# Optimization experiments

Measured on AMD Instinct MI355X. Metric: run time of the kernel, lower is better.

The kernel has to match this reference:

```python
import jax, jax.numpy as jnp
import numpy as np

BS, T, C, H, W = 2, 3, 256, 48, 48
NH, NP, NL = 8, 4, 3
DH = C // NH
HW = H * W
LQ = T * HW


def conv2d(x, w, b):
    # x: (N,C,H,W), w: (O,I,3,3), padding=1 (SAME)
    y = jax.lax.conv_general_dilated(x, w, (1, 1), 'SAME',
                                     dimension_numbers=('NCHW', 'OIHW', 'NCHW'))
    return y + b[None, :, None, None]


def grid_sample(img, grid, align_corners, padding_mode):
    # img: (B,C,Hi,Wi); grid: (B,Hg,Wg,2) in [-1,1], last dim = (x,y)
    B, Ch, Hi, Wi = img.shape
    gx, gy = grid[..., 0], grid[..., 1]
    if align_corners:
        x = (gx + 1.0) * 0.5 * (Wi - 1)
        y = (gy + 1.0) * 0.5 * (Hi - 1)
    else:
        x = ((gx + 1.0) * Wi - 1.0) * 0.5
        y = ((gy + 1.0) * Hi - 1.0) * 0.5
    if padding_mode == 'border':
        x = jnp.clip(x, 0.0, Wi - 1)
        y = jnp.clip(y, 0.0, Hi - 1)
    x0 = jnp.floor(x); y0 = jnp.floor(y)
    x1 = x0 + 1.0; y1 = y0 + 1.0
    wx1 = x - x0; wx0 = 1.0 - wx1
    wy1 = y - y0; wy0 = 1.0 - wy1
    imgf = img.reshape(B, Ch, Hi * Wi)

    def gather(xi, yi):
        xc = jnp.clip(xi, 0, Wi - 1).astype(jnp.int32)
        yc = jnp.clip(yi, 0, Hi - 1).astype(jnp.int32)
        flat = (yc * Wi + xc).reshape(B, 1, -1)
        g = jnp.take_along_axis(imgf, flat, axis=2).reshape(B, Ch, *xi.shape[1:])
        if padding_mode == 'zeros':
            valid = ((xi >= 0) & (xi <= Wi - 1) & (yi >= 0) & (yi <= Hi - 1))
            g = g * valid[:, None].astype(img.dtype)
        return g

    out = (gather(x0, y0) * (wx0 * wy0)[:, None]
           + gather(x1, y0) * (wx1 * wy0)[:, None]
           + gather(x0, y1) * (wx0 * wy1)[:, None]
           + gather(x1, y1) * (wx1 * wy1)[:, None])
    return out


def warp(x, flo):
    # x: (B,C,H,W), flo: (B,2,H,W) pixel flow; border padding, align_corners=True
    B, Ch, Hh, Ww = x.shape
    gy, gx = jnp.meshgrid(jnp.arange(Hh), jnp.arange(Ww), indexing='ij')
    grid = jnp.stack([gx, gy], 0).astype(x.dtype)[None]  # (1,2,H,W)
    v = grid + flo
    vx = 2.0 * v[:, 0] / max(Ww - 1, 1) - 1.0
    vy = 2.0 * v[:, 1] / max(Hh - 1, 1) - 1.0
    g = jnp.stack([vx, vy], -1)  # (B,H,W,2)
    return grid_sample(x, g, align_corners=True, padding_mode='border')


def flow_guid_offset(flow_forward, flow_backward, off, h, w):
    # off: (N, LQ, NH, NL, NP, 2) -> add frame-to-frame flows per (query level, key level)
    N = off.shape[0]
    hw = h * w
    off = off.reshape(N, NL, hw, NH, NL, NP, 2)
    f01 = flow_forward[:, 0]; f12 = flow_forward[:, 1]
    f02 = f01 + warp(f12, f01)
    b10 = flow_backward[:, 0]; b21 = flow_backward[:, 1]
    b20 = b21 + warp(b10, b21)

    def flat(f):
        return f.transpose(0, 2, 3, 1).reshape(N, hw, 2)

    f01, f12, f02, b10, b21, b20 = map(flat, (f01, f12, f02, b10, b21, b20))
    z = jnp.zeros_like(f01)
    add = jnp.stack([
        jnp.stack([z, f01, f02], axis=2),
        jnp.stack([b10, z, f12], axis=2),
        jnp.stack([b20, b21, z], axis=2)], axis=1)  # (N, 3, hw, 3, 2)
    off = off + add[:, :, :, None, :, None, :]
    return off.reshape(N, NL * hw, NH, NL, NP, 2)


def setup_inputs():
    key = jax.random.key(0)
    ks = jax.random.split(key, 12)
    query = jax.random.normal(ks[0], (BS, T, C, H, W), dtype=jnp.float32)
    input_flatten = jax.random.normal(ks[1], (BS, T, C, H, W), dtype=jnp.float32)
    reference_points = jax.random.uniform(ks[2], (BS, LQ, NL, 2), dtype=jnp.float32)
    input_spatial_shapes = jnp.array([[H, W]] * NL, dtype=jnp.int32)
    input_level_start_index = jnp.array([0, HW, 2 * HW], dtype=jnp.int32)
    input_padding_mask = jnp.zeros((BS, LQ), dtype=bool)
    flow_forward = 3.0 * jax.random.normal(ks[3], (BS, 2, 2, H, W), dtype=jnp.float32)
    flow_backward = 3.0 * jax.random.normal(ks[4], (BS, 2, 2, H, W), dtype=jnp.float32)
    # sampling_offsets bias init (as in _reset_parameters)
    thetas = np.arange(NH) * (2.0 * np.pi / NH)
    g = np.stack([np.cos(thetas), np.sin(thetas)], -1)
    g = g / np.abs(g).max(-1, keepdims=True)
    g = np.tile(g.reshape(NH, 1, 1, 2), (1, NL, NP, 1))
    g = g * (np.arange(NP) + 1).reshape(1, 1, NP, 1)
    b_off = jnp.asarray(g.reshape(-1), dtype=jnp.float32)
    fan = 1.0 / np.sqrt(C * 9)
    w_off = 0.01 * jax.random.normal(ks[5], (NH * NL * NP * 2, C, 3, 3), dtype=jnp.float32)
    w_attn = 0.01 * jax.random.normal(ks[6], (NH * NL * NP, C, 3, 3), dtype=jnp.float32)
    b_attn = jnp.zeros((NH * NL * NP,), dtype=jnp.float32)
    w_val = fan * jax.random.normal(ks[7], (C, C, 3, 3), dtype=jnp.float32)
    b_val = jnp.zeros((C,), dtype=jnp.float32)
    w_out = fan * jax.random.normal(ks[8], (C, C, 3, 3), dtype=jnp.float32)
    b_out = jnp.zeros((C,), dtype=jnp.float32)
    return {'query': query, 'reference_points': reference_points,
            'input_flatten': input_flatten,
            'input_spatial_shapes': input_spatial_shapes,
            'input_level_start_index': input_level_start_index,
            'input_padding_mask': input_padding_mask,
            'flow_forward': flow_forward, 'flow_backward': flow_backward,
            'w_off': w_off, 'b_off': b_off, 'w_attn': w_attn, 'b_attn': b_attn,
            'w_val': w_val, 'b_val': b_val, 'w_out': w_out, 'b_out': b_out}


def reference(query, reference_points, input_flatten, input_spatial_shapes,
              input_level_start_index, input_padding_mask, flow_forward,
              flow_backward, w_off, b_off, w_attn, b_attn, w_val, b_val,
              w_out, b_out):
    bs, t, c, h, w = query.shape
    q2d = query.reshape(bs * t, c, h, w)
    value = conv2d(input_flatten.reshape(bs * t, c, h, w), w_val, b_val)
    off = conv2d(q2d, w_off, b_off)
    attn = conv2d(q2d, w_attn, b_attn)

    def to_seq(x2d, ch):
        return x2d.reshape(bs, t, ch, h * w).transpose(0, 1, 3, 2).reshape(bs, t * h * w, ch)

    value = to_seq(value, c)
    off = to_seq(off, NH * NL * NP * 2)
    attn = to_seq(attn, NH * NL * NP)
    value = jnp.where(input_padding_mask[..., None], 0.0, value)
    value = value.reshape(bs, t * h * w, NH, DH)
    off = off.reshape(bs, LQ, NH, NL, NP, 2)
    off = flow_guid_offset(flow_forward, flow_backward, off, h, w)
    attn = jax.nn.softmax(attn.reshape(bs, LQ, NH, NL * NP), axis=-1)
    attn = attn.reshape(bs, LQ, NH, NL, NP)
    # offset normalizer: (W_l, H_l) per level
    norm = jnp.stack([input_spatial_shapes[:, 1], input_spatial_shapes[:, 0]], -1).astype(off.dtype)
    loc = reference_points[:, :, None, :, None, :] + off / norm[None, None, None, :, None, :]
    grids = 2.0 * loc - 1.0  # (bs, LQ, NH, NL, NP, 2)
    # values per level -> (NL*bs*NH, DH, h, w)
    v = value.reshape(bs, NL, h, w, NH, DH).transpose(1, 0, 4, 5, 2, 3).reshape(NL * bs * NH, DH, h, w)
    g = grids.transpose(3, 0, 2, 1, 4, 5).reshape(NL * bs * NH, LQ, NP, 2)
    sampled = grid_sample(v, g, align_corners=False, padding_mode='zeros')  # (NL*bs*NH, DH, LQ, NP)
    sampled = sampled.reshape(NL, bs, NH, DH, LQ, NP)
    out = jnp.einsum('lnhdqp,nqhlp->nqhd', sampled, attn).reshape(bs, LQ, c)
    out = out.reshape(bs, t, h * w, c).transpose(0, 1, 3, 2).reshape(bs * t, c, h, w)
    return conv2d(out, w_out, b_out)
```

## Files before the change

kernel.cpp:

```cpp
#include <hip/hip_runtime.h>
#include <hip/hip_bf16.h>

#define BS   2
#define T    3
#define CCH  256
#define HH   48
#define WW   48
#define NH   8
#define NP   4
#define NL   3
#define DH   32
#define HWP  (HH*WW)
#define LQ   (T*HWP)
#define NIMG (BS*T)

typedef short v8s __attribute__((ext_vector_type(8)));
typedef float v4f __attribute__((ext_vector_type(4)));
typedef float v2f __attribute__((ext_vector_type(2)));
typedef unsigned int v2u __attribute__((ext_vector_type(2)));
typedef unsigned int v4u __attribute__((ext_vector_type(4)));

__device__ __forceinline__ unsigned short f2b(float f) {
    unsigned u = __float_as_uint(f);
    return (unsigned short)((u + 0x7FFFu + ((u >> 16) & 1u)) >> 16);
}

#define GLOAD_LDS16(gp, lp) \
    __builtin_amdgcn_global_load_lds((const __attribute__((address_space(1))) unsigned int*)(const void*)(gp), \
                                     (__attribute__((address_space(3))) unsigned int*)(void*)(lp), 16, 0, 0)

#define LDS_SLAB  32768
#define LDS_ZROW  69632
#define LDS_TOTAL 69760

__device__ __forceinline__ int xcd_swz(int p, int n) {
    int q = n >> 3, r = n & 7;
    int xcd = p & 7, j = p >> 3;
    return (xcd < r ? xcd * (q + 1) : r * (q + 1) + (xcd - r) * q) + j;
}

#define NB_FLOW 18
#define NB_WCVT 800
#define NB_TCVT 6912
#define WP0 (256*256)
#define WP1 (288*256)

__global__ __launch_bounds__(256) void prep_kernel(
    const float* __restrict__ ff, const float* __restrict__ fb,
    float* __restrict__ addb,
    const float* __restrict__ w_val, const float* __restrict__ w_off,
    const float* __restrict__ w_attn, const float* __restrict__ w_out,
    unsigned short* __restrict__ Wb_val, unsigned short* __restrict__ Wb_oa,
    unsigned short* __restrict__ Wb_out,
    const float* __restrict__ inputf, const float* __restrict__ query,
    unsigned short* __restrict__ inb_v, unsigned short* __restrict__ inb_q)
{
    __shared__ float lds[32][33];
    const int b = blockIdx.x;
    const int tid = threadIdx.x;

    if (b < NB_FLOW) {
        int idx = b * 256 + tid;
        int n = idx / HWP, pix = idx % HWP;
        int y = pix / WW, x = pix % WW;

        auto F = [&](const float* base, int i, int c, int p) {
            return base[n * (2*2*HWP) + i * (2*HWP) + c * HWP + p];
        };

        float f01x = F(ff,0,0,pix), f01y = F(ff,0,1,pix);
        float f12x = F(ff,1,0,pix), f12y = F(ff,1,1,pix);
        float b10x = F(fb,0,0,pix), b10y = F(fb,0,1,pix);
        float b21x = F(fb,1,0,pix), b21y = F(fb,1,1,pix);

        auto bil = [&](const float* base, int i, float fx, float fy, float* ox, float* oy) {
            float vx = (float)x + fx;
            float vy = (float)y + fy;
            float gx = 2.0f * vx / (float)(WW - 1) - 1.0f;
            float gy = 2.0f * vy / (float)(HH - 1) - 1.0f;
            float px = (gx + 1.0f) * 0.5f * (float)(WW - 1);
            float py = (gy + 1.0f) * 0.5f * (float)(HH - 1);
            px = fminf(fmaxf(px, 0.0f), (float)(WW - 1));
            py = fminf(fmaxf(py, 0.0f), (float)(HH - 1));
            float x0f = floorf(px), y0f = floorf(py);
            float wx1 = px - x0f, wx0 = 1.0f - wx1;
            float wy1 = py - y0f, wy0 = 1.0f - wy1;
            int xi0 = (int)x0f, yi0 = (int)y0f;
            int xc0 = min(max(xi0, 0), WW-1), xc1 = min(max(xi0+1, 0), WW-1);
            int yc0 = min(max(yi0, 0), HH-1), yc1 = min(max(yi0+1, 0), HH-1);
            float r[2];
            #pragma unroll
            for (int c = 0; c < 2; ++c) {
                float v00 = F(base, i, c, yc0*WW + xc0);
                float v10 = F(base, i, c, yc0*WW + xc1);
                float v01 = F(base, i, c, yc1*WW + xc0);
                float v11 = F(base, i, c, yc1*WW + xc1);
                r[c] = v00*(wx0*wy0) + v10*(wx1*wy0) + v01*(wx0*wy1) + v11*(wx1*wy1);
            }
            *ox = r[0]; *oy = r[1];
        };

        float wfx, wfy; bil(ff, 1, f01x, f01y, &wfx, &wfy);
        float f02x = f01x + wfx, f02y = f01y + wfy;
        float wbx, wby; bil(fb, 0, b21x, b21y, &wbx, &wby);
        float b20x = b21x + wbx, b20y = b21y + wby;

        float* A = addb + n * (3*HWP*6) + pix * 6;
        const int TS = HWP * 6;
        A[0] = 0.f;   A[1] = 0.f;   A[2] = f01x; A[3] = f01y; A[4] = f02x; A[5] = f02y;
        A[TS+0] = b10x; A[TS+1] = b10y; A[TS+2] = 0.f; A[TS+3] = 0.f; A[TS+4] = f12x; A[TS+5] = f12y;
        A[2*TS+0] = b20x; A[2*TS+1] = b20y; A[2*TS+2] = b21x; A[2*TS+3] = b21y; A[2*TS+4] = 0.f; A[2*TS+5] = 0.f;
    } else if (b < NB_FLOW + NB_WCVT) {
        int idx = (b - NB_FLOW) * 256 + tid;
        if (idx < WP0) {
            int oc = idx >> 8, ic = idx & 255;
            const float* sp = w_val + ((size_t)oc * 256 + ic) * 9;
            #pragma unroll
            for (int j = 0; j < 9; ++j)
                Wb_val[(size_t)j * WP0 + oc * 256 + ic] = f2b(sp[j]);
        } else if (idx < WP0 + WP1) {
            int p3 = idx - WP0;
            int oc = p3 >> 8, ic = p3 & 255;
            const float* sp = (oc < 192)
                ? (w_off  + ((size_t)oc * 256 + ic) * 9)
                : (w_attn + ((size_t)(oc - 192) * 256 + ic) * 9);
            #pragma unroll
            for (int j = 0; j < 9; ++j)
                Wb_oa[(size_t)j * WP1 + oc * 256 + ic] = f2b(sp[j]);
        } else {
            int p3 = idx - WP0 - WP1;
            int oc = p3 >> 8, ic = p3 & 255;
            const float* sp = w_out + ((size_t)oc * 256 + ic) * 9;
            #pragma unroll
            for (int j = 0; j < 9; ++j)
                Wb_out[(size_t)j * WP0 + oc * 256 + ic] = f2b(sp[j]);
        }
    } else {
        int rem = b - NB_FLOW - NB_WCVT;
        int which = rem / 3456;
        int r2 = rem % 3456;
        int px0 = (r2 % 72) * 32;
        int ic0 = ((r2 / 72) % 8) * 32;
        int img = r2 / (72 * 8);
        const float* src = which ? query : inputf;
        unsigned short* dst = which ? inb_q : inb_v;
        #pragma unroll
        for (int s = 0; s < 4; ++s) {
            int icl = (tid >> 5) + s * 8, pxl = tid & 31;
            lds[icl][pxl] = src[((size_t)img * 256 + ic0 + icl) * HWP + px0 + pxl];
        }
        __syncthreads();
        #pragma unroll
        for (int s = 0; s < 4; ++s) {
            int pxl = (tid >> 5) + s * 8, icl = tid & 31;
            dst[((size_t)img * HWP + px0 + pxl) * 256 + ic0 + icl] = f2b(lds[icl][pxl]);
        }
    }
}

template<int NM>
__device__ __forceinline__ void conv_body(
    int cls, int s, int c_lo, int c_hi,
    const char* inIc, const char* Wbc, int Mpad, int oc0, int pxb, int img,
    const float* bias_a, const float* bias_off, const float* bias_attn,
    unsigned short* Vout, float* offb, float* attnb, float* outp,
    const unsigned char* mask, char* lds)
{
    const int tid  = threadIdx.x;
    const int lane = tid & 63;
    const int wv   = tid >> 6;

    const int r0   = pxb / 48;
    const int rlo  = (r0 > 0) ? (r0 - 1) : 0;
    const int pxlo = rlo * 48;

    const int lrow8 = lane >> 3;
    const int lcol  = lane & 7;

    const int rowl = lane & 15;
    const int g    = lane >> 4;
    const int keyx = (rowl & 7) << 4;
    const int aoff0 = ((wv >> 1) * (16 * NM) + rowl) * 128;
    const int pxw   = pxb + (wv & 1) * 64;
    int ypx[4], xpx[4];
    #pragma unroll
    for (int p = 0; p < 4; ++p) {
        int px = pxw + p * 16 + rowl;
        ypx[p] = px / 48;
        xpx[p] = px % 48;
    }
    int ocr_[NM];
    #pragma unroll
    for (int j = 0; j < NM; ++j) ocr_[j] = j * 32 + wv * 8 + lrow8;

    v4f acc[NM][4];
    #pragma unroll
    for (int m = 0; m < NM; ++m)
        #pragma unroll
        for (int p = 0; p < 4; ++p)
            #pragma unroll
            for (int e = 0; e < 4; ++e) acc[m][p][e] = 0.f;

    for (int c = c_lo; c < c_hi; ++c) {
        const int ic0b = c * 128;

        #pragma unroll
        for (int rr = 0; rr < 9; ++rr) {
            int pe  = rr * 32 + wv * 8 + lrow8;
            int gpx = pxlo + pe;
            if (gpx > 2303) gpx = 2303;
            GLOAD_LDS16(inIc + (size_t)gpx * 512 + ic0b + ((lcol ^ (pe & 7)) << 4),
                        lds + LDS_SLAB + (rr * 32 + wv * 8) * 128);
        }
        #pragma unroll
        for (int j = 0; j < NM; ++j) {
            GLOAD_LDS16(Wbc + (size_t)(oc0 + ocr_[j]) * 512 + ic0b + ((lcol ^ (ocr_[j] & 7)) << 4),
                        lds + (j * 32 + wv * 8) * 128);
        }
        asm volatile("s_waitcnt vmcnt(0) lgkmcnt(0)" ::: "memory");
        __builtin_amdgcn_s_barrier();

        for (int k = 0; k < 9; ++k) {
            const int dy = k / 3 - 1, dx = k % 3 - 1;
            const int cur = k & 1;
            if (k < 8) {
                const char* wk1 = Wbc + (size_t)(k + 1) * Mpad * 512;
                #pragma unroll
                for (int j = 0; j < NM; ++j) {
                    GLOAD_LDS16(wk1 + (size_t)(oc0 + ocr_[j]) * 512 + ic0b + ((lcol ^ (ocr_[j] & 7)) << 4),
                                lds + (cur ^ 1) * 16384 + (j * 32 + wv * 8) * 128);
                }
                if (NM == 4) { asm volatile("s_waitcnt vmcnt(4)" ::: "memory"); }
                else         { asm volatile("s_waitcnt vmcnt(3)" ::: "memory"); }
            } else {
                asm volatile("s_waitcnt vmcnt(0)" ::: "memory");
            }
            __builtin_amdgcn_s_barrier();

            int bbase[4], bkey[4];
            #pragma unroll
            for (int p = 0; p < 4; ++p) {
                int ys = ypx[p] + dy, xs = xpx[p] + dx;
                bool val = ((unsigned)ys < 48u) && ((unsigned)xs < 48u);
                int pe = ys * 48 + xs - pxlo;
                bbase[p] = val ? (LDS_SLAB + pe * 128) : LDS_ZROW;
                bkey[p]  = val ? ((pe & 7) << 4) : 0;
            }

            #pragma unroll
            for (int kk = 0; kk < 2; ++kk) {
                const int col = kk * 64 + g * 16;
                v8s a[NM], bfr[4];
                #pragma unroll
                for (int m = 0; m < NM; ++m)
                    a[m] = *(const v8s*)(lds + cur * 16384 + aoff0 + m * 2048 + (col ^ keyx));
                #pragma unroll
                for (int p = 0; p < 4; ++p)
                    bfr[p] = *(const v8s*)(lds + bbase[p] + (col ^ bkey[p]));
                #pragma unroll
                for (int m = 0; m < NM; ++m)
                    #pragma unroll
                    for (int p = 0; p < 4; ++p)
                        acc[m][p] = __builtin_amdgcn_mfma_f32_16x16x32_bf16(a[m], bfr[p], acc[m][p], 0, 0, 0);
            }
            __builtin_amdgcn_s_barrier();
        }
    }

    const int n = img / T, t = img % T;
    const int ocw = oc0 + (wv >> 1) * (16 * NM);

    #pragma unroll
    for (int p = 0; p < 4; ++p) {
        const int px_f = pxw + p * 16 + rowl;
        const int q = t * HWP + px_f;
        bool mk = (cls == 0) ? (mask[n * LQ + q] != 0) : false;
        #pragma unroll
        for (int m = 0; m < NM; ++m) {
            const int oc_f = ocw + m * 16 + g * 4;
            if (cls == 0) {
                unsigned short o[4];
                #pragma unroll
                for (int r = 0; r < 4; ++r) {
                    float v = acc[m][p][r] + bias_a[oc_f + r];
                    if (mk) v = 0.f;
                    o[r] = f2b(v);
                }
                int head = oc_f >> 5, d0 = oc_f & 31;
                v2u pk;
                pk[0] = (unsigned)o[0] | ((unsigned)o[1] << 16);
                pk[1] = (unsigned)o[2] | ((unsigned)o[3] << 16);
                *(v2u*)(Vout + (((size_t)(t * BS + n) * NH + head) * HWP + px_f) * 32 + d0) = pk;
            } else if (cls == 1) {
                if (oc_f < 192) {
                    v4f v;
                    #pragma unroll
                    for (int r = 0; r < 4; ++r) v[r] = acc[m][p][r] + bias_off[oc_f + r];
                    *(v4f*)(offb + ((size_t)n * LQ + q) * 192 + oc_f) = v;
                } else {
                    v4f v;
                    #pragma unroll
                    for (int r = 0; r < 4; ++r) v[r] = acc[m][p][r] + bias_attn[oc_f - 192 + r];
                    *(v4f*)(attnb + ((size_t)n * LQ + q) * 96 + (oc_f - 192)) = v;
                }
            } else {
                #pragma unroll
                for (int r = 0; r < 4; ++r) {
                    float v = acc[m][p][r] + ((s == 0) ? bias_a[oc_f + r] : 0.f);
                    atomicAdd(&outp[((size_t)img * CCH + oc_f + r) * HWP + px_f], v);
                }
            }
        }
    }
}

__global__ __launch_bounds__(256) void convbig(
    int phase,
    const unsigned short* __restrict__ in_a,
    const unsigned short* __restrict__ in_b,
    const unsigned short* __restrict__ Wb_a,
    const unsigned short* __restrict__ Wb_b,
    const float* __restrict__ bias_a,
    const float* __restrict__ bias_off,
    const float* __restrict__ bias_attn,
    unsigned short* __restrict__ Vout,
    float* __restrict__ offb,
    float* __restrict__ attnb,
    float* __restrict__ outp,
    const unsigned char* __restrict__ mask)
{
    __shared__ __align__(16) char lds[LDS_TOTAL];

    const int tid = threadIdx.x;
    if (tid < 8) {
        v8s z;
        #pragma unroll
        for (int j = 0; j < 8; ++j) z[j] = 0;
        *(v8s*)(lds + LDS_ZROW + tid * 16) = z;
    }

    const int p_phys = blockIdx.x;
    int b;
    if (p_phys < 216) b = xcd_swz(p_phys, 216);
    else if (phase == 0) b = 216 + xcd_swz(p_phys - 216, 324);
    else b = 216 + xcd_swz(p_phys - 216, 216);

    int cls, mt, nt, img, Mpad, c_lo, c_hi, s, oc0;
    const unsigned short *inb, *Wb;
    if (phase == 0) {
        s = 0; c_lo = 0; c_hi = 4;
        if (b < 216) { cls = 0; mt = b % 2; int r = b / 2; nt = r % 18; img = r / 18;
                       inb = in_a; Wb = Wb_a; Mpad = 256; oc0 = mt * 128; }
        else { b -= 216; cls = 1; mt = b % 3; int r = b / 3; nt = r % 18; img = r / 18;
               inb = in_b; Wb = Wb_b; Mpad = 288; oc0 = mt * 96; }
    } else {
        cls = 3; s = b / 216; b = b % 216;
        c_lo = 2 * s; c_hi = c_lo + 2;
        mt = b % 2; int r = b / 2; nt = r % 18; img = r / 18;
        inb = in_a; Wb = Wb_a; Mpad = 256; oc0 = mt * 128;
    }

    const int pxb = nt * 128;
    const char* inIc = (const char*)(inb + (size_t)img * HWP * 256);
    const char* Wbc  = (const char*)Wb;

    if (cls == 1) {
        conv_body<3>(cls, s, c_lo, c_hi, inIc, Wbc, Mpad, oc0, pxb, img,
                     bias_a, bias_off, bias_attn, Vout, offb, attnb, outp, mask, lds);
    } else {
        conv_body<4>(cls, s, c_lo, c_hi, inIc, Wbc, Mpad, oc0, pxb, img,
                     bias_a, bias_off, bias_attn, Vout, offb, attnb, outp, mask, lds);
    }
}

__global__ __launch_bounds__(256) void sample_kernel(
    const unsigned short* __restrict__ V,
    const float* __restrict__ offb,
    const float* __restrict__ attnb,
    const float* __restrict__ addb,
    const float* __restrict__ refp,
    unsigned short* __restrict__ midb)
{
    const int tid = threadIdx.x;
    const int gid = tid >> 2, li = tid & 3;
    const int lb = xcd_swz(blockIdx.x, (BS * LQ * NH) / 64);
    const int pair = lb * 64 + gid;
    const int head = pair & 7;
    const int nq = pair >> 3;
    const int n = nq / LQ, q = nq % LQ;
    const int t = q / HWP, pix = q % HWP;

    const float* al = attnb + ((size_t)n * LQ + q) * 96 + head * 12;
    float lg[12];
    {
        v4f t0 = *(const v4f*)al, t1 = *(const v4f*)(al + 4), t2 = *(const v4f*)(al + 8);
        #pragma unroll
        for (int j = 0; j < 4; ++j) { lg[j] = t0[j]; lg[4+j] = t1[j]; lg[8+j] = t2[j]; }
    }
    const float* ofp = offb + ((size_t)n * LQ + q) * 192 + head * 24;
    float of[24];
    #pragma unroll
    for (int j = 0; j < 6; ++j) {
        v4f v = *(const v4f*)(ofp + j * 4);
        #pragma unroll
        for (int e = 0; e < 4; ++e) of[j*4+e] = v[e];
    }
    const float* rpp = refp + ((size_t)n * LQ + q) * 6;
    const float* adp = addb + ((size_t)n * 3 * HWP + t * HWP + pix) * 6;
    float rp[6], ad[6];
    #pragma unroll
    for (int j = 0; j < 3; ++j) {
        v2f r = *(const v2f*)(rpp + j * 2);
        v2f a = *(const v2f*)(adp + j * 2);
        rp[j*2] = r[0]; rp[j*2+1] = r[1];
        ad[j*2] = a[0]; ad[j*2+1] = a[1];
    }

    float m = lg[0];
    #pragma unroll
    for (int j = 1; j < 12; ++j) m = fmaxf(m, lg[j]);
    float s = 0.f;
    #pragma unroll
    for (int j = 0; j < 12; ++j) { lg[j] = expf(lg[j] - m); s += lg[j]; }
    float inv = 1.0f / s;
    #pragma unroll
    for (int j = 0; j < 12; ++j) lg[j] *= inv;

    float acc[8];
    #pragma unroll
    for (int e = 0; e < 8; ++e) acc[e] = 0.f;

    #pragma unroll
    for (int l = 0; l < 3; ++l) {
        float refx = rp[l*2+0], refy = rp[l*2+1];
        float addx = ad[l*2+0], addy = ad[l*2+1];
        const unsigned short* Vi =
            V + (size_t)((l * BS + n) * NH + head) * HWP * DH + li * 8;
        #pragma unroll
        for (int p = 0; p < 4; ++p) {
            float ox = of[(l*4+p)*2+0] + addx;
            float oy = of[(l*4+p)*2+1] + addy;
            float locx = refx + ox * (1.0f/48.0f);
            float locy = refy + oy * (1.0f/48.0f);
            float gx = 2.0f*locx - 1.0f;
            float gy = 2.0f*locy - 1.0f;
            float pxf = ((gx + 1.0f) * 48.0f - 1.0f) * 0.5f;
            float pyf = ((gy + 1.0f) * 48.0f - 1.0f) * 0.5f;
            float x0f = floorf(pxf), y0f = floorf(pyf);
            float wx1 = pxf - x0f, wx0 = 1.0f - wx1;
            float wy1 = pyf - y0f, wy0 = 1.0f - wy1;
            int xi0 = (int)x0f, yi0 = (int)y0f;
            bool vx0 = (x0f >= 0.0f)     && (x0f <= 47.0f);
            bool vx1 = (x0f+1.f >= 0.0f) && (x0f+1.f <= 47.0f);
            bool vy0 = (y0f >= 0.0f)     && (y0f <= 47.0f);
            bool vy1 = (y0f+1.f >= 0.0f) && (y0f+1.f <= 47.0f);
            int xc0 = min(max(xi0, 0), 47),   xc1 = min(max(xi0+1, 0), 47);
            int yc0 = min(max(yi0, 0), 47),   yc1 = min(max(yi0+1, 0), 47);
            float aw = lg[l*4+p];
            float w00 = (vx0 && vy0) ? wx0*wy0*aw : 0.f;
            float w10 = (vx1 && vy0) ? wx1*wy0*aw : 0.f;
            float w01 = (vx0 && vy1) ? wx0*wy1*aw : 0.f;
            float w11 = (vx1 && vy1) ? wx1*wy1*aw : 0.f;
            v4u u00 = *(const v4u*)(Vi + (yc0*WW + xc0)*DH);
            v4u u10 = *(const v4u*)(Vi + (yc0*WW + xc1)*DH);
            v4u u01 = *(const v4u*)(Vi + (yc1*WW + xc0)*DH);
            v4u u11 = *(const v4u*)(Vi + (yc1*WW + xc1)*DH);
            #pragma unroll
            for (int cc = 0; cc < 4; ++cc) {
                v4u u = (cc == 0) ? u00 : (cc == 1) ? u10 : (cc == 2) ? u01 : u11;
                float w = (cc == 0) ? w00 : (cc == 1) ? w10 : (cc == 2) ? w01 : w11;
                #pragma unroll
                for (int e = 0; e < 4; ++e) {
                    acc[e*2+0] += w * __uint_as_float(u[e] << 16);
                    acc[e*2+1] += w * __uint_as_float(u[e] & 0xFFFF0000u);
                }
            }
        }
    }

    v4u pk;
    #pragma unroll
    for (int e = 0; e < 4; ++e)
        pk[e] = (unsigned)f2b(acc[e*2+0]) | ((unsigned)f2b(acc[e*2+1]) << 16);
    *(v4u*)(midb + ((size_t)(n * T + t) * HWP + pix) * 256 + head * 32 + li * 8) = pk;
}

extern "C" void kernel_launch(void* const* d_in, const int* in_sizes, int n_in,
                              void* d_out, int out_size, void* d_ws, size_t ws_size,
                              hipStream_t stream) {
    const float* query  = (const float*)d_in[0];
    const float* refp   = (const float*)d_in[1];
    const float* inputf = (const float*)d_in[2];
    const unsigned char* mask = (const unsigned char*)d_in[5];
    const float* ff     = (const float*)d_in[6];
    const float* fb     = (const float*)d_in[7];
    const float* w_off  = (const float*)d_in[8];
    const float* b_off  = (const float*)d_in[9];
    const float* w_attn = (const float*)d_in[10];
    const float* b_attn = (const float*)d_in[11];
    const float* w_val  = (const float*)d_in[12];
    const float* b_val  = (const float*)d_in[13];
    const float* w_out  = (const float*)d_in[14];
    const float* b_out  = (const float*)d_in[15];

    char* w = (char*)d_ws;
    float* offb  = (float*)w;           w += (size_t)BS*LQ*192*4;
    float* attnb = (float*)w;           w += (size_t)BS*LQ*96*4;
    float* addb  = (float*)w;           w += (size_t)BS*3*HWP*6*4;
    unsigned short* V      = (unsigned short*)w; w += (size_t)48*HWP*DH*2;
    unsigned short* inb_q  = (unsigned short*)w; w += (size_t)NIMG*HWP*256*2;
    unsigned short* inb_v  = (unsigned short*)w; w += (size_t)NIMG*HWP*256*2;
    unsigned short* midb   = inb_v;
    unsigned short* Wb_val = (unsigned short*)w; w += (size_t)9*256*256*2;
    unsigned short* Wb_oa  = (unsigned short*)w; w += (size_t)9*288*256*2;
    unsigned short* Wb_out = (unsigned short*)w; w += (size_t)9*256*256*2;
    float* outp = (float*)d_out;

    hipMemsetAsync(outp, 0, (size_t)NIMG * CCH * HWP * 4, stream);

    prep_kernel<<<NB_FLOW + NB_WCVT + NB_TCVT, 256, 0, stream>>>(
        ff, fb, addb, w_val, w_off, w_attn, w_out,
        Wb_val, Wb_oa, Wb_out, inputf, query, inb_v, inb_q);

    convbig<<<540, 256, 0, stream>>>(0, inb_v, inb_q, Wb_val, Wb_oa,
                                     b_val, b_off, b_attn,
                                     V, offb, attnb, nullptr, mask);

    sample_kernel<<<(BS*LQ*NH)/64, 256, 0, stream>>>(V, offb, attnb, addb, refp, midb);

    convbig<<<432, 256, 0, stream>>>(1, midb, nullptr, Wb_out, nullptr,
                                     b_out, nullptr, nullptr,
                                     nullptr, nullptr, nullptr, outp, nullptr);
}
```

Baseline: 139.5 us.

## Pre-pack conv weights in MFMA fragment order and load A operands directly from global

```diff
diff --git a/kernel.cpp b/kernel.cpp
--- a/kernel.cpp
+++ b/kernel.cpp
@@ -29,9 +29,8 @@
     __builtin_amdgcn_global_load_lds((const __attribute__((address_space(1))) unsigned int*)(const void*)(gp), \
                                      (__attribute__((address_space(3))) unsigned int*)(void*)(lp), 16, 0, 0)
 
-#define LDS_SLAB  32768
-#define LDS_ZROW  69632
-#define LDS_TOTAL 69760
+#define LDS_ZROW  36864
+#define LDS_TOTAL 36992
 
 __device__ __forceinline__ int xcd_swz(int p, int n) {
     int q = n >> 3, r = n & 7;
@@ -44,6 +43,16 @@
 #define NB_TCVT 6912
 #define WP0 (256*256)
 #define WP1 (288*256)
+
+__device__ __forceinline__ void wfrag_store(
+    unsigned short* dst, int Mp, int oc, int ic, int k, float v)
+{
+    int c = ic >> 6, kk = (ic >> 5) & 1, g = (ic >> 3) & 3, j8 = ic & 7;
+    int rowl = oc & 15, ob = oc >> 4;
+    int lane = (g << 4) | rowl;
+    size_t idx = ((((size_t)(k * 4 + c) * (Mp >> 4) + ob) * 2 + kk) * 64 + lane) * 8 + j8;
+    dst[idx] = f2b(v);
+}
 
 __global__ __launch_bounds__(256) void prep_kernel(
     const float* __restrict__ ff, const float* __restrict__ fb,
@@ -117,7 +126,7 @@
             const float* sp = w_val + ((size_t)oc * 256 + ic) * 9;
             #pragma unroll
             for (int j = 0; j < 9; ++j)
-                Wb_val[(size_t)j * WP0 + oc * 256 + ic] = f2b(sp[j]);
+                wfrag_store(Wb_val, 256, oc, ic, j, sp[j]);
         } else if (idx < WP0 + WP1) {
             int p3 = idx - WP0;
             int oc = p3 >> 8, ic = p3 & 255;
@@ -126,14 +135,14 @@
                 : (w_attn + ((size_t)(oc - 192) * 256 + ic) * 9);
             #pragma unroll
             for (int j = 0; j < 9; ++j)
-                Wb_oa[(size_t)j * WP1 + oc * 256 + ic] = f2b(sp[j]);
+                wfrag_store(Wb_oa, 288, oc, ic, j, sp[j]);
         } else {
             int p3 = idx - WP0 - WP1;
             int oc = p3 >> 8, ic = p3 & 255;
             const float* sp = w_out + ((size_t)oc * 256 + ic) * 9;
             #pragma unroll
             for (int j = 0; j < 9; ++j)
-                Wb_out[(size_t)j * WP0 + oc * 256 + ic] = f2b(sp[j]);
+                wfrag_store(Wb_out, 256, oc, ic, j, sp[j]);
         }
     } else {
         int rem = b - NB_FLOW - NB_WCVT;
@@ -161,7 +170,7 @@
 template<int NM>
 __device__ __forceinline__ void conv_body(
     int cls, int s, int c_lo, int c_hi,
-    const char* inIc, const char* Wbc, int Mpad, int oc0, int pxb, int img,
+    const char* inIc, const char* WbF, int Mpad, int oc0, int pxb, int img,
     const float* bias_a, const float* bias_off, const float* bias_attn,
     unsigned short* Vout, float* offb, float* attnb, float* outp,
     const unsigned char* mask, char* lds)
@@ -179,9 +188,9 @@
 
     const int rowl = lane & 15;
     const int g    = lane >> 4;
-    const int keyx = (rowl & 7) << 4;
-    const int aoff0 = ((wv >> 1) * (16 * NM) + rowl) * 128;
-    const int pxw   = pxb + (wv & 1) * 64;
+    const int pxw  = pxb + (wv & 1) * 64;
+    const int ob0  = (oc0 >> 4) + (wv >> 1) * NM;
+    const int obn  = Mpad >> 4;
     int ypx[4], xpx[4];
     #pragma unroll
     for (int p = 0; p < 4; ++p) {
@@ -189,9 +198,6 @@
         ypx[p] = px / 48;
         xpx[p] = px % 48;
     }
-    int ocr_[NM];
-    #pragma unroll
-    for (int j = 0; j < NM; ++j) ocr_[j] = j * 32 + wv * 8 + lrow8;
 
     v4f acc[NM][4];
     #pragma unroll
@@ -204,56 +210,42 @@
     for (int c = c_lo; c < c_hi; ++c) {
         const int ic0b = c * 128;
 
+        __syncthreads();
         #pragma unroll
         for (int rr = 0; rr < 9; ++rr) {
             int pe  = rr * 32 + wv * 8 + lrow8;
             int gpx = pxlo + pe;
             if (gpx > 2303) gpx = 2303;
             GLOAD_LDS16(inIc + (size_t)gpx * 512 + ic0b + ((lcol ^ (pe & 7)) << 4),
-                        lds + LDS_SLAB + (rr * 32 + wv * 8) * 128);
-        }
-        #pragma unroll
-        for (int j = 0; j < NM; ++j) {
-            GLOAD_LDS16(Wbc + (size_t)(oc0 + ocr_[j]) * 512 + ic0b + ((lcol ^ (ocr_[j] & 7)) << 4),
-                        lds + (j * 32 + wv * 8) * 128);
+                        lds + (rr * 32 + wv * 8) * 128);
         }
         asm volatile("s_waitcnt vmcnt(0) lgkmcnt(0)" ::: "memory");
         __builtin_amdgcn_s_barrier();
 
         for (int k = 0; k < 9; ++k) {
+            const char* ak = WbF + ((size_t)(k * 4 + c) * obn) * 2048 + lane * 16;
+            v8s a[NM][2];
+            #pragma unroll
+            for (int m = 0; m < NM; ++m)
+                #pragma unroll
+                for (int kk = 0; kk < 2; ++kk)
+                    a[m][kk] = *(const v8s*)(ak + (size_t)((ob0 + m) * 2 + kk) * 1024);
+
             const int dy = k / 3 - 1, dx = k % 3 - 1;
-            const int cur = k & 1;
-            if (k < 8) {
-                const char* wk1 = Wbc + (size_t)(k + 1) * Mpad * 512;
-                #pragma unroll
-                for (int j = 0; j < NM; ++j) {
-                    GLOAD_LDS16(wk1 + (size_t)(oc0 + ocr_[j]) * 512 + ic0b + ((lcol ^ (ocr_[j] & 7)) << 4),
-                                lds + (cur ^ 1) * 16384 + (j * 32 + wv * 8) * 128);
-                }
-                if (NM == 4) { asm volatile("s_waitcnt vmcnt(4)" ::: "memory"); }
-                else         { asm volatile("s_waitcnt vmcnt(3)" ::: "memory"); }
-            } else {
-                asm volatile("s_waitcnt vmcnt(0)" ::: "memory");
-            }
-            __builtin_amdgcn_s_barrier();
-
             int bbase[4], bkey[4];
             #pragma unroll
             for (int p = 0; p < 4; ++p) {
                 int ys = ypx[p] + dy, xs = xpx[p] + dx;
                 bool val = ((unsigned)ys < 48u) && ((unsigned)xs < 48u);
                 int pe = ys * 48 + xs - pxlo;
-                bbase[p] = val ? (LDS_SLAB + pe * 128) : LDS_ZROW;
+                bbase[p] = val ? (pe * 128) : LDS_ZROW;
                 bkey[p]  = val ? ((pe & 7) << 4) : 0;
             }
 
             #pragma unroll
             for (int kk = 0; kk < 2; ++kk) {
                 const int col = kk * 64 + g * 16;
-                v8s a[NM], bfr[4];
-                #pragma unroll
-                for (int m = 0; m < NM; ++m)
-                    a[m] = *(const v8s*)(lds + cur * 16384 + aoff0 + m * 2048 + (col ^ keyx));
+                v8s bfr[4];
                 #pragma unroll
                 for (int p = 0; p < 4; ++p)
                     bfr[p] = *(const v8s*)(lds + bbase[p] + (col ^ bkey[p]));
@@ -261,9 +253,8 @@
                 for (int m = 0; m < NM; ++m)
                     #pragma unroll
                     for (int p = 0; p < 4; ++p)
-                        acc[m][p] = __builtin_amdgcn_mfma_f32_16x16x32_bf16(a[m], bfr[p], acc[m][p], 0, 0, 0);
+                        acc[m][p] = __builtin_amdgcn_mfma_f32_16x16x32_bf16(a[m][kk], bfr[p], acc[m][p], 0, 0, 0);
             }
-            __builtin_amdgcn_s_barrier();
         }
     }
 
@@ -362,13 +353,13 @@
 
     const int pxb = nt * 128;
     const char* inIc = (const char*)(inb + (size_t)img * HWP * 256);
-    const char* Wbc  = (const char*)Wb;
+    const char* WbFc = (const char*)Wb;
 
     if (cls == 1) {
-        conv_body<3>(cls, s, c_lo, c_hi, inIc, Wbc, Mpad, oc0, pxb, img,
+        conv_body<3>(cls, s, c_lo, c_hi, inIc, WbFc, Mpad, oc0, pxb, img,
                      bias_a, bias_off, bias_attn, Vout, offb, attnb, outp, mask, lds);
     } else {
-        conv_body<4>(cls, s, c_lo, c_hi, inIc, Wbc, Mpad, oc0, pxb, img,
+        conv_body<4>(cls, s, c_lo, c_hi, inIc, WbFc, Mpad, oc0, pxb, img,
                      bias_a, bias_off, bias_attn, Vout, offb, attnb, outp, mask, lds);
     }
 }
```

After: 234.4 us. +68.1%, slower.
